# Kernel optimization log

Measured on AMD Instinct MI355X. Metric: run time of the kernel, lower is better.

The kernel has to match this reference:

```python
import jax, jax.numpy as jnp
import numpy as np
from jax import lax

# static config matching init_kwargs
H, W = 128, 128
THETA_RES, RHO_RES = 1.0, 1.0
C_IN, C_OUT = 64, 64
A = int(np.round(180.0 / THETA_RES))            # num angle bins = 180
R = int(np.ceil(np.sqrt(H * H + W * W) / RHO_RES))  # num rho bins = 182


def _make_rho_idx():
    # rho bin index for every (angle, pixel); pixels flattened h-major (h*W + w)
    th = np.arange(A, dtype=np.float64) * THETA_RES * np.pi / 180.0
    hh, ww = np.meshgrid(np.arange(H), np.arange(W), indexing='ij')
    xs = (ww - W / 2.0).ravel()
    ys = (hh - H / 2.0).ravel()
    r = np.round((xs[None, :] * np.cos(th)[:, None]
                  + ys[None, :] * np.sin(th)[:, None]) / RHO_RES).astype(np.int32)
    r = r + R // 2
    return np.clip(r, 0, R - 1)  # [A, H*W] int32


def dht(x, rho_idx):
    # Hough scatter: [N,C,H,W] -> [N,C,A,R]
    N, C, h, w = x.shape
    xf = x.reshape(N * C, h * w).T  # [HW, NC]

    def step(_, idx_a):
        acc = jax.ops.segment_sum(xf, idx_a, num_segments=R)  # [R, NC]
        return None, acc

    _, ht = lax.scan(step, None, rho_idx)       # [A, R, NC]
    return ht.transpose(2, 0, 1).reshape(N, C, A, R)


def idht(ht, rho_idx):
    # inverse Hough gather (transpose of dht): [N,C,A,R] -> [N,C,H,W]
    N, C, a, r = ht.shape
    hf = ht.reshape(N * C, a, r).transpose(1, 0, 2)  # [A, NC, R]

    def step(acc, args):
        ht_a, idx_a = args
        return acc + ht_a[:, idx_a], None  # gather along rho -> [NC, HW]

    acc0 = jnp.zeros((N * C, H * W), ht.dtype)
    acc, _ = lax.scan(step, acc0, (hf, rho_idx))
    return acc.reshape(N, C, H, W)


def conv91_relu(x, w, b, groups):
    # Conv2d kernel (9,1), padding (4,0), stride 1 + ReLU
    y = lax.conv_general_dilated(x, w, (1, 1), [(4, 4), (0, 0)],
                                 dimension_numbers=('NCHW', 'OIHW', 'NCHW'),
                                 feature_group_count=groups)
    return jax.nn.relu(y + b[None, :, None, None])


def setup_inputs():
    key = jax.random.key(0)
    ks = jax.random.split(key, 7)
    N = 4
    x = jax.random.normal(ks[0], (N, C_IN, H, W), dtype=jnp.float32)
    s1 = 1.0 / np.sqrt(9.0)
    s2 = 1.0 / np.sqrt(9.0 * C_IN)
    w1 = jax.random.normal(ks[1], (C_IN, 1, 9, 1), jnp.float32) * s1
    b1 = jax.random.normal(ks[2], (C_IN,), jnp.float32) * 0.01
    w2 = jax.random.normal(ks[3], (C_IN, C_IN, 9, 1), jnp.float32) * s2
    b2 = jax.random.normal(ks[4], (C_IN,), jnp.float32) * 0.01
    w3 = jax.random.normal(ks[5], (C_OUT, C_IN, 9, 1), jnp.float32) * s2
    b3 = jax.random.normal(ks[6], (C_OUT,), jnp.float32) * 0.01
    rho_idx = jnp.asarray(_make_rho_idx())  # [A, H*W] int32, precomputed buffer
    return {"x": x, "rho_idx": rho_idx, "w1": w1, "b1": b1,
            "w2": w2, "b2": b2, "w3": w3, "b3": b3}


def reference(x, rho_idx, w1, b1, w2, b2, w3, b3):
    out = dht(x, rho_idx)                       # [N,C,A,R]
    out = conv91_relu(out, w1, b1, groups=C_IN) # grouped (9,1) conv
    out = conv91_relu(out, w2, b2, groups=1)
    out = conv91_relu(out, w3, b3, groups=1)
    return idht(out, rho_idx)                   # [N,C_OUT,H,W]
```

## Files before the change

### kernel.cpp

```cpp
#include <hip/hip_runtime.h>

typedef unsigned short ushort_t;
typedef __attribute__((ext_vector_type(8))) short short8;
typedef __attribute__((ext_vector_type(4))) float float4v;

#define HW 16384
#define A_BINS 180
#define R_BINS 182
#define AP 188
#define CCH 64
#define NB 4
#define NC 256
#define MROWS (A_BINS * R_BINS)
#define MPROWS (AP * R_BINS)
#define PADPX HW
#define PLSTRIDE 17664

static __device__ __forceinline__ float b2f(ushort_t u) {
    union { unsigned u32; float f; } c; c.u32 = ((unsigned)u) << 16; return c.f;
}
static __device__ __forceinline__ float u2f(unsigned u) {
    union { unsigned u32; float f; } c; c.u32 = u; return c.f;
}
static __device__ __forceinline__ ushort_t f2b(float f) {
    union { float f; unsigned u; } c; c.f = f;
    unsigned r = c.u + 0x7fffu + ((c.u >> 16) & 1u);
    return (ushort_t)(r >> 16);
}
static __device__ __forceinline__ float4v cvt4(uint2 u) {
    return (float4v){u2f(u.x << 16), u2f(u.x & 0xffff0000u),
                     u2f(u.y << 16), u2f(u.y & 0xffff0000u)};
}

__global__ __launch_bounds__(256) void k_transpose(const float* __restrict__ x,
                                                   ushort_t* __restrict__ xT) {
    __shared__ float tile[64][65];
    int t = threadIdx.x, lane = t & 63, g = t >> 6;
    int pBase = blockIdx.x * 64;
    int ncBase = blockIdx.y * 64;
#pragma unroll
    for (int i = 0; i < 16; ++i) {
        int ncl = g + i * 4;
        tile[ncl][lane] = x[(size_t)(ncBase + ncl) * HW + pBase + lane];
    }
    __syncthreads();
#pragma unroll
    for (int i = 0; i < 16; ++i) {
        int pl = g + i * 4;
        xT[(size_t)(pBase + pl) * 256 + ncBase + lane] = f2b(tile[lane][pl]);
    }
}

__global__ __launch_bounds__(256) void k_setup(ushort_t* __restrict__ ht0,
                                               ushort_t* __restrict__ bufA,
                                               ushort_t* __restrict__ bufB,
                                               const float* __restrict__ w2,
                                               const float* __restrict__ w3,
                                               ushort_t* __restrict__ w2b,
                                               ushort_t* __restrict__ w3b,
                                               ushort_t* __restrict__ xT) {
    int blk = blockIdx.x, t = threadIdx.x;
    if (blk == 312) {
        if (t < 64) ((uint2*)(xT + (size_t)PADPX * NC))[t] = (uint2){0u, 0u};
        return;
    }
    if (blk < 24) {
        int b = blk >> 3, j = blk & 7;
        int ap = (j < 4) ? j : (184 + (j - 4));
        ushort_t* base = (b == 0 ? ht0 : (b == 1 ? bufA : bufB));
        uint4* p = (uint4*)(base + (size_t)ap * (R_BINS * NC));
        int n16 = R_BINS * NC / 8;
        for (int i = t; i < n16; i += 256) p[i] = (uint4){0, 0, 0, 0};
        return;
    }
    int rep = blk - 24;
    const float* w = (rep >= 144) ? w3 : w2;
    ushort_t* wb = (rep >= 144) ? w3b : w2b;
    int idx = (rep % 144) * 256 + t;
    int j = idx & 7;
    int lane = (idx >> 3) & 63;
    int cot = (idx >> 9) & 3;
    int h = (idx >> 11) & 1;
    int k = idx >> 12;
    int co = cot * 16 + (lane & 15);
    int ci = h * 32 + (lane >> 4) * 8 + j;
    wb[idx] = f2b(w[(co * 64 + ci) * 9 + k]);
}

__global__ __launch_bounds__(256) void k_csr(const int* __restrict__ rho,
                                             int* __restrict__ offs,
                                             ushort_t* __restrict__ plist) {
    __shared__ int hist[4][R_BINS];
    __shared__ int tot[R_BINS];
    __shared__ int offl[R_BINS + 1];
    __shared__ int cur[4][R_BINS];
    __shared__ ushort_t sp[PLSTRIDE];
    int a = blockIdx.x, t = threadIdx.x, lane = t & 63, wv = t >> 6;
    for (int i = t; i < 4 * R_BINS; i += 256) ((int*)hist)[i] = 0;
    __syncthreads();
    const int* rA = rho + (size_t)a * HW;
#pragma unroll 4
    for (int i = 0; i < 64; ++i) {
        int r = rA[t + i * 256];
        atomicAdd(&hist[wv][r], 1);
    }
    __syncthreads();
    if (t < R_BINS) tot[t] = hist[0][t] + hist[1][t] + hist[2][t] + hist[3][t];
    __syncthreads();
    if (wv == 0) {
        int b0 = lane * 3;
        int c0 = (b0     < R_BINS) ? ((tot[b0]     + 7) & ~7) : 0;
        int c1 = (b0 + 1 < R_BINS) ? ((tot[b0 + 1] + 7) & ~7) : 0;
        int c2 = (b0 + 2 < R_BINS) ? ((tot[b0 + 2] + 7) & ~7) : 0;
        int sum = c0 + c1 + c2, inc = sum;
#pragma unroll
        for (int d = 1; d < 64; d <<= 1) {
            int vv = __shfl_up(inc, d);
            if (lane >= d) inc += vv;
        }
        int excl = inc - sum;
        if (b0     < R_BINS) offl[b0]     = excl;
        if (b0 + 1 < R_BINS) offl[b0 + 1] = excl + c0;
        if (b0 + 2 < R_BINS) offl[b0 + 2] = excl + c0 + c1;
        if (lane == 63) offl[R_BINS] = inc;
    }
    __syncthreads();
    if (t < R_BINS) {
        int b = offl[t];
        cur[0][t] = b; b += hist[0][t];
        cur[1][t] = b; b += hist[1][t];
        cur[2][t] = b; b += hist[2][t];
        cur[3][t] = b;
    }
    if (t <= R_BINS) offs[a * (R_BINS + 1) + t] = offl[t];
    __syncthreads();
#pragma unroll 4
    for (int i = 0; i < 64; ++i) {
        int p = t + i * 256;
        int r = rA[p];
        int pos = atomicAdd(&cur[wv][r], 1);
        sp[pos] = (ushort_t)p;
    }
    __syncthreads();
    if (t < R_BINS) {
        int base = offl[t] + tot[t];
        int pend = offl[t + 1];
        for (int k = base; k < pend; ++k) sp[k] = (ushort_t)PADPX;
    }
    __syncthreads();
    int len = offl[R_BINS];
    const uint4* spv = (const uint4*)sp;
    uint4* plv = (uint4*)(plist + (size_t)a * PLSTRIDE);
    for (int i = t; i < len / 8; i += 256) plv[i] = spv[i];
}

__global__ __launch_bounds__(256, 4) void k_dht_g5(const ushort_t* __restrict__ xT,
                                                   const int* __restrict__ offs,
                                                   const ushort_t* __restrict__ plist,
                                                   ushort_t* __restrict__ ht0) {
    int ax = blockIdx.x;
    int a = ax >> 1, half = ax & 1;
    int part = blockIdx.y;
    int t = threadIdx.x, lane = t & 63, wv = t >> 6;
    int wslot = part * 4 + wv;
    int nl = lane & 15;
    unsigned lhb = (unsigned)nl * 16;
    unsigned shsel = (lane & 16) ? 16u : 0u;
    const char* xh = (const char*)xT + half * 256;
    const uint4* plq = (const uint4*)(plist + (size_t)a * PLSTRIDE);
    const int* offA = offs + a * (R_BINS + 1);
    size_t obase = (size_t)(a + 4) * (R_BINS * NC) + half * 128;
    for (int r = wslot; r < R_BINS; r += 64) {
        int off = __builtin_amdgcn_readfirstlane(offA[r]);
        int end = __builtin_amdgcn_readfirstlane(offA[r + 1]);
        float4v acc0 = (float4v){0.f, 0.f, 0.f, 0.f};
        float4v acc1 = (float4v){0.f, 0.f, 0.f, 0.f};
        int j = off;
        if (j < end) {
            uint4 w = plq[j >> 3];
            for (;;) {
                int jn = j + 8;
                uint4 wn = (uint4){0u, 0u, 0u, 0u};
                bool more = jn < end;
                if (more) wn = plq[jn >> 3];
                {
                    unsigned we = (lane & 32) ? w.y : w.x;
                    unsigned ps = (we >> shsel) & 0xffffu;
                    uint4 u = *(const uint4*)(xh + ((size_t)ps << 9) + lhb);
                    acc0 += cvt4((uint2){u.x, u.y});
                    acc1 += cvt4((uint2){u.z, u.w});
                }
                {
                    unsigned we = (lane & 32) ? w.w : w.z;
                    unsigned ps = (we >> shsel) & 0xffffu;
                    uint4 u = *(const uint4*)(xh + ((size_t)ps << 9) + lhb);
                    acc0 += cvt4((uint2){u.x, u.y});
                    acc1 += cvt4((uint2){u.z, u.w});
                }
                if (!more) break;
                w = wn; j = jn;
            }
        }
#pragma unroll
        for (int c = 0; c < 4; ++c) {
            acc0[c] += __shfl_xor(acc0[c], 16);
            acc1[c] += __shfl_xor(acc1[c], 16);
        }
#pragma unroll
        for (int c = 0; c < 4; ++c) {
            acc0[c] += __shfl_xor(acc0[c], 32);
            acc1[c] += __shfl_xor(acc1[c], 32);
        }
        if (lane < 16) {
            uint4 o;
            o.x = (unsigned)f2b(acc0[0]) | ((unsigned)f2b(acc0[1]) << 16);
            o.y = (unsigned)f2b(acc0[2]) | ((unsigned)f2b(acc0[3]) << 16);
            o.z = (unsigned)f2b(acc1[0]) | ((unsigned)f2b(acc1[1]) << 16);
            o.w = (unsigned)f2b(acc1[2]) | ((unsigned)f2b(acc1[3]) << 16);
            *(uint4*)(ht0 + obase + (size_t)r * NC + nl * 8) = o;
        }
    }
}

__global__ __launch_bounds__(256) void k_conv1(const ushort_t* __restrict__ ht0,
                                               const float* __restrict__ w1,
                                               const float* __restrict__ b1,
                                               ushort_t* __restrict__ bufA) {
    int t = threadIdx.x, c = t & 63;
    int r = blockIdx.x;
    int a0 = blockIdx.y * 30;
    float wr[9];
#pragma unroll
    for (int k = 0; k < 9; ++k) wr[k] = w1[c * 9 + k];
    float bb = b1[c];
    const ushort_t* ip = ht0 + ((size_t)a0 * R_BINS + r) * NC + t;
    float v[38];
#pragma unroll
    for (int j = 0; j < 38; ++j) v[j] = b2f(ip[(size_t)j * (R_BINS * NC)]);
    ushort_t* op = bufA + ((size_t)(a0 + 4) * R_BINS + r) * NC + t;
#pragma unroll
    for (int i = 0; i < 30; ++i) {
        float s = bb;
#pragma unroll
        for (int k = 0; k < 9; ++k) s = fmaf(v[i + k], wr[k], s);
        op[(size_t)i * (R_BINS * NC)] = f2b(fmaxf(s, 0.f));
    }
}

__global__ __launch_bounds__(256) void k_gemm(const ushort_t* __restrict__ in,
                                              const ushort_t* __restrict__ wb,
                                              const float* __restrict__ bias,
                                              ushort_t* __restrict__ out,
                                              int outRowOff) {
    __shared__ ushort_t Bs[36864];
    int t = threadIdx.x, lane = t & 63, wv = t >> 6;
    {
        const uint4* src = (const uint4*)wb;
        uint4* dst = (uint4*)Bs;
        for (int i = t; i < 36864 / 8; i += 256) dst[i] = src[i];
    }
    __syncthreads();
    int m = lane & 15, q = lane >> 4;
    int n = blockIdx.y;
    int rowBase = blockIdx.x * 256 + wv * 64;
    const ushort_t* inN = in + n * 64;
    size_t rof[4];
#pragma unroll
    for (int tl = 0; tl < 4; ++tl) {
        int row = rowBase + tl * 16 + m;
        int rowc = row < MROWS ? row : (MROWS - 1);
        rof[tl] = (size_t)rowc * NC;
    }
    float4v acc[4][4];
#pragma unroll
    for (int tl = 0; tl < 4; ++tl)
#pragma unroll
        for (int i = 0; i < 4; ++i) acc[tl][i] = (float4v){0.f, 0.f, 0.f, 0.f};

#pragma unroll
    for (int k = 0; k < 9; ++k) {
#pragma unroll
        for (int h = 0; h < 2; ++h) {
            const ushort_t* base = inN + (size_t)k * (R_BINS * NC) + h * 32 + q * 8;
            short8 af0 = *(const short8*)(base + rof[0]);
            short8 af1 = *(const short8*)(base + rof[1]);
            short8 af2 = *(const short8*)(base + rof[2]);
            short8 af3 = *(const short8*)(base + rof[3]);
            const ushort_t* bl = Bs + (size_t)((k * 2 + h) * 4) * 512 + lane * 8;
            short8 b0 = *(const short8*)(bl);
            short8 b1v = *(const short8*)(bl + 512);
            short8 b2v = *(const short8*)(bl + 1024);
            short8 b3v = *(const short8*)(bl + 1536);
            acc[0][0] = __builtin_amdgcn_mfma_f32_16x16x32_bf16(af0, b0, acc[0][0], 0, 0, 0);
            acc[0][1] = __builtin_amdgcn_mfma_f32_16x16x32_bf16(af0, b1v, acc[0][1], 0, 0, 0);
            acc[0][2] = __builtin_amdgcn_mfma_f32_16x16x32_bf16(af0, b2v, acc[0][2], 0, 0, 0);
            acc[0][3] = __builtin_amdgcn_mfma_f32_16x16x32_bf16(af0, b3v, acc[0][3], 0, 0, 0);
            acc[1][0] = __builtin_amdgcn_mfma_f32_16x16x32_bf16(af1, b0, acc[1][0], 0, 0, 0);
            acc[1][1] = __builtin_amdgcn_mfma_f32_16x16x32_bf16(af1, b1v, acc[1][1], 0, 0, 0);
            acc[1][2] = __builtin_amdgcn_mfma_f32_16x16x32_bf16(af1, b2v, acc[1][2], 0, 0, 0);
            acc[1][3] = __builtin_amdgcn_mfma_f32_16x16x32_bf16(af1, b3v, acc[1][3], 0, 0, 0);
            acc[2][0] = __builtin_amdgcn_mfma_f32_16x16x32_bf16(af2, b0, acc[2][0], 0, 0, 0);
            acc[2][1] = __builtin_amdgcn_mfma_f32_16x16x32_bf16(af2, b1v, acc[2][1], 0, 0, 0);
            acc[2][2] = __builtin_amdgcn_mfma_f32_16x16x32_bf16(af2, b2v, acc[2][2], 0, 0, 0);
            acc[2][3] = __builtin_amdgcn_mfma_f32_16x16x32_bf16(af2, b3v, acc[2][3], 0, 0, 0);
            acc[3][0] = __builtin_amdgcn_mfma_f32_16x16x32_bf16(af3, b0, acc[3][0], 0, 0, 0);
            acc[3][1] = __builtin_amdgcn_mfma_f32_16x16x32_bf16(af3, b1v, acc[3][1], 0, 0, 0);
            acc[3][2] = __builtin_amdgcn_mfma_f32_16x16x32_bf16(af3, b2v, acc[3][2], 0, 0, 0);
            acc[3][3] = __builtin_amdgcn_mfma_f32_16x16x32_bf16(af3, b3v, acc[3][3], 0, 0, 0);
        }
    }

    ushort_t* outN = out + n * 64;
#pragma unroll
    for (int tl = 0; tl < 4; ++tl) {
#pragma unroll
        for (int cot = 0; cot < 4; ++cot) {
            int co = cot * 16 + m;
            float bv = bias[co];
#pragma unroll
            for (int i = 0; i < 4; ++i) {
                int rowD = rowBase + tl * 16 + q * 4 + i;
                float v = fmaxf(acc[tl][cot][i] + bv, 0.f);
                if (rowD < MROWS) outN[(size_t)(rowD + outRowOff) * NC + co] = f2b(v);
            }
        }
    }
}

union SharedIdht {
    int rhoL[A_BINS * 32];
    float tile[2 * 256 * 33];
};

#define IDHT_LOAD(S, ang) do { \
    int4 rv0_ = *(const int4*)&u.rhoL[(ang) * 32 + wq * 8]; \
    int4 rv1_ = *(const int4*)&u.rhoL[(ang) * 32 + wq * 8 + 4]; \
    const char* bA_ = (const char*)buf3 + (size_t)(ang) * (R_BINS * NC * 2); \
    { unsigned r_ = (unsigned)(h ? rv0_.y : rv0_.x); S[0] = *(const uint4*)(bA_ + ((size_t)r_ << 9) + lhb); } \
    { unsigned r_ = (unsigned)(h ? rv0_.w : rv0_.z); S[1] = *(const uint4*)(bA_ + ((size_t)r_ << 9) + lhb); } \
    { unsigned r_ = (unsigned)(h ? rv1_.y : rv1_.x); S[2] = *(const uint4*)(bA_ + ((size_t)r_ << 9) + lhb); } \
    { unsigned r_ = (unsigned)(h ? rv1_.w : rv1_.z); S[3] = *(const uint4*)(bA_ + ((size_t)r_ << 9) + lhb); } \
    } while (0)

#define IDHT_CONSUME(S) do { \
    _Pragma("unroll") \
    for (int p_ = 0; p_ < 4; ++p_) { \
        accv[2 * p_]     += cvt4((uint2){S[p_].x, S[p_].y}); \
        accv[2 * p_ + 1] += cvt4((uint2){S[p_].z, S[p_].w}); \
    } } while (0)

__global__ __launch_bounds__(512, 2) void k_idht(const ushort_t* __restrict__ buf3,
                                                 const int* __restrict__ rho,
                                                 float* __restrict__ outp) {
    __shared__ SharedIdht u;
    int t = threadIdx.x, lane = t & 63, wv = t >> 6;
    int grp = wv >> 2;
    int wq = wv & 3;
    int P0 = blockIdx.x * 32;
    int h = lane >> 5;
    unsigned lhb = (unsigned)(lane & 31) * 16;
    for (int i = t; i < A_BINS * 32; i += 512) {
        int a = i >> 5, px = i & 31;
        u.rhoL[a * 32 + px] = rho[(size_t)a * HW + P0 + px];
    }
    __syncthreads();
    float4v accv[8];
#pragma unroll
    for (int i = 0; i < 8; ++i) accv[i] = (float4v){0.f, 0.f, 0.f, 0.f};
    int a0 = grp * 90;

    uint4 S0[4], S1[4], S2[4];
    IDHT_LOAD(S0, a0);
    IDHT_LOAD(S1, a0 + 1);
    IDHT_LOAD(S2, a0 + 2);
    for (int k = 0; k <= 84; k += 3) {
        IDHT_CONSUME(S0); IDHT_LOAD(S0, a0 + k + 3);
        IDHT_CONSUME(S1); IDHT_LOAD(S1, a0 + k + 4);
        IDHT_CONSUME(S2); IDHT_LOAD(S2, a0 + k + 5);
    }
    IDHT_CONSUME(S0);
    IDHT_CONSUME(S1);
    IDHT_CONSUME(S2);

    __syncthreads();
#pragma unroll
    for (int p = 0; p < 4; ++p) {
        int px = wq * 8 + p * 2 + h;
#pragma unroll
        for (int cc = 0; cc < 8; ++cc)
            u.tile[(size_t)grp * 8448 + ((lane & 31) * 8 + cc) * 33 + px] =
                accv[2 * p + (cc >> 2)][cc & 3];
    }
    __syncthreads();
    int px = t & 31, nc0 = t >> 5;
    float* on = outp + P0 + px;
#pragma unroll
    for (int k = 0; k < 16; ++k) {
        int nc = nc0 + k * 16;
        on[(size_t)nc * HW] = u.tile[nc * 33 + px] + u.tile[8448 + nc * 33 + px];
    }
}

extern "C" void kernel_launch(void* const* d_in, const int* in_sizes, int n_in,
                              void* d_out, int out_size, void* d_ws, size_t ws_size,
                              hipStream_t stream) {
    const float* x   = (const float*)d_in[0];
    const int*   rho = (const int*)d_in[1];
    const float* w1  = (const float*)d_in[2];
    const float* b1  = (const float*)d_in[3];
    const float* w2  = (const float*)d_in[4];
    const float* b2  = (const float*)d_in[5];
    const float* w3  = (const float*)d_in[6];
    const float* b3  = (const float*)d_in[7];
    float* outp = (float*)d_out;

    char* ws = (char*)d_ws;
    size_t off = 0;
    auto alloc = [&](size_t bytes) -> void* {
        void* p = ws + off;
        off = (off + bytes + 255) & ~(size_t)255;
        return p;
    };
    ushort_t* xT    = (ushort_t*)alloc((size_t)(HW + 8) * NC * 2);
    ushort_t* ht0   = (ushort_t*)alloc((size_t)AP * R_BINS * NC * 2);
    ushort_t* bufA  = (ushort_t*)alloc((size_t)AP * R_BINS * NC * 2);
    ushort_t* bufB  = (ushort_t*)alloc((size_t)AP * R_BINS * NC * 2);
    ushort_t* buf3  = (ushort_t*)alloc((size_t)A_BINS * R_BINS * NC * 2);
    ushort_t* w2b   = (ushort_t*)alloc(36864 * 2);
    ushort_t* w3b   = (ushort_t*)alloc(36864 * 2);
    int*      offs  = (int*)alloc((size_t)A_BINS * (R_BINS + 1) * 4);
    ushort_t* plist = (ushort_t*)alloc((size_t)A_BINS * PLSTRIDE * 2);

    k_transpose<<<dim3(256, 4), 256, 0, stream>>>(x, xT);
    k_setup<<<313, 256, 0, stream>>>(ht0, bufA, bufB, w2, w3, w2b, w3b, xT);
    k_csr<<<A_BINS, 256, 0, stream>>>(rho, offs, plist);
    k_dht_g5<<<dim3(360, 16), 256, 0, stream>>>(xT, offs, plist, ht0);
    k_conv1<<<dim3(R_BINS, 6), 256, 0, stream>>>(ht0, w1, b1, bufA);
    k_gemm<<<dim3(128, NB), 256, 0, stream>>>(bufA, w2b, b2, bufB, 728);
    k_gemm<<<dim3(128, NB), 256, 0, stream>>>(bufB, w3b, b3, buf3, 0);
    k_idht<<<dim3(512), 512, 0, stream>>>(buf3, rho, outp);
}
```

Baseline: 315.9 us.

## Fuse prep kernels, use packed f32 adds, reorder DHT/IDHT block mapping

```diff
diff --git a/kernel.cpp b/kernel.cpp
--- a/kernel.cpp
+++ b/kernel.cpp
@@ -3,6 +3,7 @@
 typedef unsigned short ushort_t;
 typedef __attribute__((ext_vector_type(8))) short short8;
 typedef __attribute__((ext_vector_type(4))) float float4v;
+typedef __attribute__((ext_vector_type(2))) float float2v;
 
 #define HW 16384
 #define A_BINS 180
@@ -27,91 +28,103 @@
     unsigned r = c.u + 0x7fffu + ((c.u >> 16) & 1u);
     return (ushort_t)(r >> 16);
 }
+static __device__ __forceinline__ void pkacc(float2v& a, float lo, float hi) {
+    float2v b; b.x = lo; b.y = hi;
+    asm("v_pk_add_f32 %0, %1, %0" : "+v"(a) : "v"(b));
+}
 static __device__ __forceinline__ float4v cvt4(uint2 u) {
     return (float4v){u2f(u.x << 16), u2f(u.x & 0xffff0000u),
                      u2f(u.y << 16), u2f(u.y & 0xffff0000u)};
 }
 
-__global__ __launch_bounds__(256) void k_transpose(const float* __restrict__ x,
-                                                   ushort_t* __restrict__ xT) {
-    __shared__ float tile[64][65];
-    int t = threadIdx.x, lane = t & 63, g = t >> 6;
-    int pBase = blockIdx.x * 64;
-    int ncBase = blockIdx.y * 64;
-#pragma unroll
-    for (int i = 0; i < 16; ++i) {
-        int ncl = g + i * 4;
-        tile[ncl][lane] = x[(size_t)(ncBase + ncl) * HW + pBase + lane];
-    }
-    __syncthreads();
-#pragma unroll
-    for (int i = 0; i < 16; ++i) {
-        int pl = g + i * 4;
-        xT[(size_t)(pBase + pl) * 256 + ncBase + lane] = f2b(tile[lane][pl]);
-    }
-}
-
-__global__ __launch_bounds__(256) void k_setup(ushort_t* __restrict__ ht0,
-                                               ushort_t* __restrict__ bufA,
-                                               ushort_t* __restrict__ bufB,
-                                               const float* __restrict__ w2,
-                                               const float* __restrict__ w3,
-                                               ushort_t* __restrict__ w2b,
-                                               ushort_t* __restrict__ w3b,
-                                               ushort_t* __restrict__ xT) {
+union PrepShared {
+    float tile[64][65];
+    struct {
+        int hist[4][R_BINS];
+        int tot[R_BINS];
+        int offl[R_BINS + 1];
+        int cur[4][R_BINS];
+        ushort_t sp[PLSTRIDE];
+    } c;
+};
+
+__global__ __launch_bounds__(256) void k_prep(const float* __restrict__ x,
+                                              ushort_t* __restrict__ xT,
+                                              ushort_t* __restrict__ ht0,
+                                              ushort_t* __restrict__ bufA,
+                                              ushort_t* __restrict__ bufB,
+                                              const float* __restrict__ w2,
+                                              const float* __restrict__ w3,
+                                              ushort_t* __restrict__ w2b,
+                                              ushort_t* __restrict__ w3b,
+                                              const int* __restrict__ rho,
+                                              int* __restrict__ offs,
+                                              ushort_t* __restrict__ plist) {
+    __shared__ PrepShared u;
     int blk = blockIdx.x, t = threadIdx.x;
-    if (blk == 312) {
-        if (t < 64) ((uint2*)(xT + (size_t)PADPX * NC))[t] = (uint2){0u, 0u};
+    if (blk < 1024) {
+        int lane = t & 63, g = t >> 6;
+        int pBase = (blk & 255) * 64;
+        int ncBase = (blk >> 8) * 64;
+#pragma unroll
+        for (int i = 0; i < 16; ++i) {
+            int ncl = g + i * 4;
+            u.tile[ncl][lane] = x[(size_t)(ncBase + ncl) * HW + pBase + lane];
+        }
+        __syncthreads();
+#pragma unroll
+        for (int i = 0; i < 16; ++i) {
+            int pl = g + i * 4;
+            xT[(size_t)(pBase + pl) * 256 + ncBase + lane] = f2b(u.tile[lane][pl]);
+        }
         return;
     }
-    if (blk < 24) {
-        int b = blk >> 3, j = blk & 7;
-        int ap = (j < 4) ? j : (184 + (j - 4));
-        ushort_t* base = (b == 0 ? ht0 : (b == 1 ? bufA : bufB));
-        uint4* p = (uint4*)(base + (size_t)ap * (R_BINS * NC));
-        int n16 = R_BINS * NC / 8;
-        for (int i = t; i < n16; i += 256) p[i] = (uint4){0, 0, 0, 0};
+    if (blk < 1337) {
+        int sblk = blk - 1024;
+        if (sblk == 312) {
+            if (t < 64) ((uint2*)(xT + (size_t)PADPX * NC))[t] = (uint2){0u, 0u};
+            return;
+        }
+        if (sblk < 24) {
+            int b = sblk >> 3, j = sblk & 7;
+            int ap = (j < 4) ? j : (184 + (j - 4));
+            ushort_t* base = (b == 0 ? ht0 : (b == 1 ? bufA : bufB));
+            uint4* p = (uint4*)(base + (size_t)ap * (R_BINS * NC));
+            int n16 = R_BINS * NC / 8;
+            for (int i = t; i < n16; i += 256) p[i] = (uint4){0, 0, 0, 0};
+            return;
+        }
+        int rep = sblk - 24;
+        const float* w = (rep >= 144) ? w3 : w2;
+        ushort_t* wb = (rep >= 144) ? w3b : w2b;
+        int idx = (rep % 144) * 256 + t;
+        int j = idx & 7;
+        int lane = (idx >> 3) & 63;
+        int cot = (idx >> 9) & 3;
+        int h = (idx >> 11) & 1;
+        int k = idx >> 12;
+        int co = cot * 16 + (lane & 15);
+        int ci = h * 32 + (lane >> 4) * 8 + j;
+        wb[idx] = f2b(w[(co * 64 + ci) * 9 + k]);
         return;
     }
-    int rep = blk - 24;
-    const float* w = (rep >= 144) ? w3 : w2;
-    ushort_t* wb = (rep >= 144) ? w3b : w2b;
-    int idx = (rep % 144) * 256 + t;
-    int j = idx & 7;
-    int lane = (idx >> 3) & 63;
-    int cot = (idx >> 9) & 3;
-    int h = (idx >> 11) & 1;
-    int k = idx >> 12;
-    int co = cot * 16 + (lane & 15);
-    int ci = h * 32 + (lane >> 4) * 8 + j;
-    wb[idx] = f2b(w[(co * 64 + ci) * 9 + k]);
-}
-
-__global__ __launch_bounds__(256) void k_csr(const int* __restrict__ rho,
-                                             int* __restrict__ offs,
-                                             ushort_t* __restrict__ plist) {
-    __shared__ int hist[4][R_BINS];
-    __shared__ int tot[R_BINS];
-    __shared__ int offl[R_BINS + 1];
-    __shared__ int cur[4][R_BINS];
-    __shared__ ushort_t sp[PLSTRIDE];
-    int a = blockIdx.x, t = threadIdx.x, lane = t & 63, wv = t >> 6;
-    for (int i = t; i < 4 * R_BINS; i += 256) ((int*)hist)[i] = 0;
+    int a = blk - 1337, lane = t & 63, wv = t >> 6;
+    for (int i = t; i < 4 * R_BINS; i += 256) ((int*)u.c.hist)[i] = 0;
     __syncthreads();
     const int* rA = rho + (size_t)a * HW;
 #pragma unroll 4
     for (int i = 0; i < 64; ++i) {
         int r = rA[t + i * 256];
-        atomicAdd(&hist[wv][r], 1);
-    }
-    __syncthreads();
-    if (t < R_BINS) tot[t] = hist[0][t] + hist[1][t] + hist[2][t] + hist[3][t];
+        atomicAdd(&u.c.hist[wv][r], 1);
+    }
+    __syncthreads();
+    if (t < R_BINS) u.c.tot[t] = u.c.hist[0][t] + u.c.hist[1][t] + u.c.hist[2][t] + u.c.hist[3][t];
     __syncthreads();
     if (wv == 0) {
         int b0 = lane * 3;
-        int c0 = (b0     < R_BINS) ? ((tot[b0]     + 7) & ~7) : 0;
-        int c1 = (b0 + 1 < R_BINS) ? ((tot[b0 + 1] + 7) & ~7) : 0;
-        int c2 = (b0 + 2 < R_BINS) ? ((tot[b0 + 2] + 7) & ~7) : 0;
+        int c0 = (b0     < R_BINS) ? ((u.c.tot[b0]     + 7) & ~7) : 0;
+        int c1 = (b0 + 1 < R_BINS) ? ((u.c.tot[b0 + 1] + 7) & ~7) : 0;
+        int c2 = (b0 + 2 < R_BINS) ? ((u.c.tot[b0 + 2] + 7) & ~7) : 0;
         int sum = c0 + c1 + c2, inc = sum;
 #pragma unroll
         for (int d = 1; d < 64; d <<= 1) {
@@ -119,47 +132,55 @@
             if (lane >= d) inc += vv;
         }
         int excl = inc - sum;
-        if (b0     < R_BINS) offl[b0]     = excl;
-        if (b0 + 1 < R_BINS) offl[b0 + 1] = excl + c0;
-        if (b0 + 2 < R_BINS) offl[b0 + 2] = excl + c0 + c1;
-        if (lane == 63) offl[R_BINS] = inc;
+        if (b0     < R_BINS) u.c.offl[b0]     = excl;
+        if (b0 + 1 < R_BINS) u.c.offl[b0 + 1] = excl + c0;
+        if (b0 + 2 < R_BINS) u.c.offl[b0 + 2] = excl + c0 + c1;
+        if (lane == 63) u.c.offl[R_BINS] = inc;
     }
     __syncthreads();
     if (t < R_BINS) {
-        int b = offl[t];
-        cur[0][t] = b; b += hist[0][t];
-        cur[1][t] = b; b += hist[1][t];
-        cur[2][t] = b; b += hist[2][t];
-        cur[3][t] = b;
-    }
-    if (t <= R_BINS) offs[a * (R_BINS + 1) + t] = offl[t];
+        int b = u.c.offl[t];
+        u.c.cur[0][t] = b; b += u.c.hist[0][t];
+        u.c.cur[1][t] = b; b += u.c.hist[1][t];
+        u.c.cur[2][t] = b; b += u.c.hist[2][t];
+        u.c.cur[3][t] = b;
+    }
+    if (t <= R_BINS) offs[a * (R_BINS + 1) + t] = u.c.offl[t];
     __syncthreads();
 #pragma unroll 4
     for (int i = 0; i < 64; ++i) {
         int p = t + i * 256;
         int r = rA[p];
-        int pos = atomicAdd(&cur[wv][r], 1);
-        sp[pos] = (ushort_t)p;
+        int pos = atomicAdd(&u.c.cur[wv][r], 1);
+        u.c.sp[pos] = (ushort_t)p;
     }
     __syncthreads();
     if (t < R_BINS) {
-        int base = offl[t] + tot[t];
-        int pend = offl[t + 1];
-        for (int k = base; k < pend; ++k) sp[k] = (ushort_t)PADPX;
-    }
-    __syncthreads();
-    int len = offl[R_BINS];
-    const uint4* spv = (const uint4*)sp;
+        int base = u.c.offl[t] + u.c.tot[t];
+        int pend = u.c.offl[t + 1];
+        for (int k = base; k < pend; ++k) u.c.sp[k] = (ushort_t)PADPX;
+    }
+    __syncthreads();
+    int len = u.c.offl[R_BINS];
+    const uint4* spv = (const uint4*)u.c.sp;
     uint4* plv = (uint4*)(plist + (size_t)a * PLSTRIDE);
     for (int i = t; i < len / 8; i += 256) plv[i] = spv[i];
 }
 
-__global__ __launch_bounds__(256, 4) void k_dht_g5(const ushort_t* __restrict__ xT,
+#define DHT_CONS(u) do { \
+    pkacc(ac0, u2f((u).x << 16), u2f((u).x & 0xffff0000u)); \
+    pkacc(ac1, u2f((u).y << 16), u2f((u).y & 0xffff0000u)); \
+    pkacc(ac2, u2f((u).z << 16), u2f((u).z & 0xffff0000u)); \
+    pkacc(ac3, u2f((u).w << 16), u2f((u).w & 0xffff0000u)); \
+} while (0)
+
+__global__ __launch_bounds__(256, 4) void k_dht_g6(const ushort_t* __restrict__ xT,
                                                    const int* __restrict__ offs,
                                                    const ushort_t* __restrict__ plist,
                                                    ushort_t* __restrict__ ht0) {
-    int ax = blockIdx.x;
-    int a = ax >> 1, half = ax & 1;
+    int bx = blockIdx.x;
+    int half = (bx >> 2) & 1;
+    int a = (bx >> 3) * 4 + (bx & 3);
     int part = blockIdx.y;
     int t = threadIdx.x, lane = t & 63, wv = t >> 6;
     int wslot = part * 4 + wv;
@@ -173,50 +194,44 @@
     for (int r = wslot; r < R_BINS; r += 64) {
         int off = __builtin_amdgcn_readfirstlane(offA[r]);
         int end = __builtin_amdgcn_readfirstlane(offA[r + 1]);
-        float4v acc0 = (float4v){0.f, 0.f, 0.f, 0.f};
-        float4v acc1 = (float4v){0.f, 0.f, 0.f, 0.f};
-        int j = off;
-        if (j < end) {
-            uint4 w = plq[j >> 3];
-            for (;;) {
-                int jn = j + 8;
-                uint4 wn = (uint4){0u, 0u, 0u, 0u};
-                bool more = jn < end;
-                if (more) wn = plq[jn >> 3];
-                {
-                    unsigned we = (lane & 32) ? w.y : w.x;
-                    unsigned ps = (we >> shsel) & 0xffffu;
-                    uint4 u = *(const uint4*)(xh + ((size_t)ps << 9) + lhb);
-                    acc0 += cvt4((uint2){u.x, u.y});
-                    acc1 += cvt4((uint2){u.z, u.w});
-                }
-                {
-                    unsigned we = (lane & 32) ? w.w : w.z;
-                    unsigned ps = (we >> shsel) & 0xffffu;
-                    uint4 u = *(const uint4*)(xh + ((size_t)ps << 9) + lhb);
-                    acc0 += cvt4((uint2){u.x, u.y});
-                    acc1 += cvt4((uint2){u.z, u.w});
-                }
-                if (!more) break;
-                w = wn; j = jn;
+        int ng = (end - off) >> 3;
+        float2v ac0 = (float2v){0.f, 0.f}, ac1 = (float2v){0.f, 0.f};
+        float2v ac2 = (float2v){0.f, 0.f}, ac3 = (float2v){0.f, 0.f};
+        if (ng > 0) {
+            int jq = off >> 3;
+            uint4 wi = plq[jq];
+            unsigned weA = (lane & 32) ? wi.y : wi.x;
+            unsigned weB = (lane & 32) ? wi.w : wi.z;
+            unsigned vA = (((weA >> shsel) & 0xffffu) << 9) + lhb;
+            unsigned vB = (((weB >> shsel) & 0xffffu) << 9) + lhb;
+            uint4 uA = *(const uint4*)(xh + vA);
+            uint4 uB = *(const uint4*)(xh + vB);
+            uint4 wn = (ng > 1) ? plq[jq + 1] : wi;
+            for (int g = 1; g < ng; ++g) {
+                uint4 wf = (g + 1 < ng) ? plq[jq + g + 1] : wn;
+                unsigned weA2 = (lane & 32) ? wn.y : wn.x;
+                unsigned weB2 = (lane & 32) ? wn.w : wn.z;
+                unsigned vA2 = (((weA2 >> shsel) & 0xffffu) << 9) + lhb;
+                unsigned vB2 = (((weB2 >> shsel) & 0xffffu) << 9) + lhb;
+                uint4 nA = *(const uint4*)(xh + vA2);
+                uint4 nB = *(const uint4*)(xh + vB2);
+                DHT_CONS(uA); DHT_CONS(uB);
+                uA = nA; uB = nB; wn = wf;
             }
-        }
-#pragma unroll
-        for (int c = 0; c < 4; ++c) {
-            acc0[c] += __shfl_xor(acc0[c], 16);
-            acc1[c] += __shfl_xor(acc1[c], 16);
-        }
-#pragma unroll
-        for (int c = 0; c < 4; ++c) {
-            acc0[c] += __shfl_xor(acc0[c], 32);
-            acc1[c] += __shfl_xor(acc1[c], 32);
+            DHT_CONS(uA); DHT_CONS(uB);
+        }
+        float rs[8] = {ac0.x, ac0.y, ac1.x, ac1.y, ac2.x, ac2.y, ac3.x, ac3.y};
+#pragma unroll
+        for (int c = 0; c < 8; ++c) {
+            rs[c] += __shfl_xor(rs[c], 16);
+            rs[c] += __shfl_xor(rs[c], 32);
         }
         if (lane < 16) {
             uint4 o;
-            o.x = (unsigned)f2b(acc0[0]) | ((unsigned)f2b(acc0[1]) << 16);
-            o.y = (unsigned)f2b(acc0[2]) | ((unsigned)f2b(acc0[3]) << 16);
-            o.z = (unsigned)f2b(acc1[0]) | ((unsigned)f2b(acc1[1]) << 16);
-            o.w = (unsigned)f2b(acc1[2]) | ((unsigned)f2b(acc1[3]) << 16);
+            o.x = (unsigned)f2b(rs[0]) | ((unsigned)f2b(rs[1]) << 16);
+            o.y = (unsigned)f2b(rs[2]) | ((unsigned)f2b(rs[3]) << 16);
+            o.z = (unsigned)f2b(rs[4]) | ((unsigned)f2b(rs[5]) << 16);
+            o.w = (unsigned)f2b(rs[6]) | ((unsigned)f2b(rs[7]) << 16);
             *(uint4*)(ht0 + obase + (size_t)r * NC + nl * 8) = o;
         }
     }
@@ -345,8 +360,10 @@
 #define IDHT_CONSUME(S) do { \
     _Pragma("unroll") \
     for (int p_ = 0; p_ < 4; ++p_) { \
-        accv[2 * p_]     += cvt4((uint2){S[p_].x, S[p_].y}); \
-        accv[2 * p_ + 1] += cvt4((uint2){S[p_].z, S[p_].w}); \
+        pkacc(accp[4 * p_ + 0], u2f(S[p_].x << 16), u2f(S[p_].x & 0xffff0000u)); \
+        pkacc(accp[4 * p_ + 1], u2f(S[p_].y << 16), u2f(S[p_].y & 0xffff0000u)); \
+        pkacc(accp[4 * p_ + 2], u2f(S[p_].z << 16), u2f(S[p_].z & 0xffff0000u)); \
+        pkacc(accp[4 * p_ + 3], u2f(S[p_].w << 16), u2f(S[p_].w & 0xffff0000u)); \
     } } while (0)
 
 __global__ __launch_bounds__(512, 2) void k_idht(const ushort_t* __restrict__ buf3,
@@ -356,7 +373,9 @@
     int t = threadIdx.x, lane = t & 63, wv = t >> 6;
     int grp = wv >> 2;
     int wq = wv & 3;
-    int P0 = blockIdx.x * 32;
+    int bid = blockIdx.x;
+    int tileId = (bid & 7) * 64 + (bid >> 3);
+    int P0 = tileId * 32;
     int h = lane >> 5;
     unsigned lhb = (unsigned)(lane & 31) * 16;
     for (int i = t; i < A_BINS * 32; i += 512) {
@@ -364,9 +383,9 @@
         u.rhoL[a * 32 + px] = rho[(size_t)a * HW + P0 + px];
     }
     __syncthreads();
-    float4v accv[8];
-#pragma unroll
-    for (int i = 0; i < 8; ++i) accv[i] = (float4v){0.f, 0.f, 0.f, 0.f};
+    float2v accp[16];
+#pragma unroll
+    for (int i = 0; i < 16; ++i) accp[i] = (float2v){0.f, 0.f};
     int a0 = grp * 90;
 
     uint4 S0[4], S1[4], S2[4];
@@ -389,7 +408,7 @@
 #pragma unroll
         for (int cc = 0; cc < 8; ++cc)
             u.tile[(size_t)grp * 8448 + ((lane & 31) * 8 + cc) * 33 + px] =
-                accv[2 * p + (cc >> 2)][cc & 3];
+                accp[4 * p + (cc >> 1)][cc & 1];
     }
     __syncthreads();
     int px = t & 31, nc0 = t >> 5;
@@ -431,10 +450,9 @@
     int*      offs  = (int*)alloc((size_t)A_BINS * (R_BINS + 1) * 4);
     ushort_t* plist = (ushort_t*)alloc((size_t)A_BINS * PLSTRIDE * 2);
 
-    k_transpose<<<dim3(256, 4), 256, 0, stream>>>(x, xT);
-    k_setup<<<313, 256, 0, stream>>>(ht0, bufA, bufB, w2, w3, w2b, w3b, xT);
-    k_csr<<<A_BINS, 256, 0, stream>>>(rho, offs, plist);
-    k_dht_g5<<<dim3(360, 16), 256, 0, stream>>>(xT, offs, plist, ht0);
+    k_prep<<<1517, 256, 0, stream>>>(x, xT, ht0, bufA, bufB, w2, w3, w2b, w3b,
+                                     rho, offs, plist);
+    k_dht_g6<<<dim3(360, 16), 256, 0, stream>>>(xT, offs, plist, ht0);
     k_conv1<<<dim3(R_BINS, 6), 256, 0, stream>>>(ht0, w1, b1, bufA);
     k_gemm<<<dim3(128, NB), 256, 0, stream>>>(bufA, w2b, b2, bufB, 728);
     k_gemm<<<dim3(128, NB), 256, 0, stream>>>(bufB, w3b, b3, buf3, 0);
```

After: 423.6 us. +34.1%, slower.
